# Optimization experiments

Measured on AMD Instinct MI355X. Metric: run time of the kernel, lower is better.

Reference implementation:

```python
import jax, jax.numpy as jnp
import numpy as np

N, NFEAT, NHID, NCLASS = 10000, 512, 64, 10
ALPHA = 0.2


def setup_inputs() -> dict:
    key = jax.random.key(0)
    ks = jax.random.split(key, 8)
    x = jax.random.normal(ks[0], (N, NFEAT), dtype=jnp.float32)
    adj1 = jax.random.uniform(ks[1], (N, N), dtype=jnp.float32) / N  # row-normalized-ish
    adj2 = jax.random.uniform(ks[2], (N, N), dtype=jnp.float32) / N
    # GraphConvolution params (glorot-ish scale)
    W1 = jax.random.normal(ks[3], (NFEAT, NHID), dtype=jnp.float32) * (1.0 / np.sqrt(NFEAT))
    b1 = jnp.zeros((NHID,), dtype=jnp.float32)
    W2 = jax.random.normal(ks[4], (NFEAT, NHID), dtype=jnp.float32) * (1.0 / np.sqrt(NFEAT))
    b2 = jnp.zeros((NHID,), dtype=jnp.float32)
    attn_w = jax.random.normal(ks[5], (NHID, 1), dtype=jnp.float32) * (1.0 / np.sqrt(NHID))
    cluster = jax.random.normal(ks[6], (NCLASS, NHID), dtype=jnp.float32)
    return {"x": x, "adj1": adj1, "adj2": adj2, "W1": W1, "b1": b1,
            "W2": W2, "b2": b2, "attn_w": attn_w, "cluster": cluster}


def reference(x, adj1, adj2, W1, b1, W2, b2, attn_w, cluster):
    # Two GCN branches: output = adj @ (x @ W) + b
    emb1 = adj1 @ (x @ W1) + b1  # [N, H]
    emb2 = adj2 @ (x @ W2) + b2  # [N, H]
    z = jnp.stack([emb1, emb2], axis=1)            # [N, 2, H]
    # tiny 2-way attention fusion
    w = z @ attn_w                                  # [N, 2, 1]
    beta = jax.nn.softmax(w, axis=1)                # softmax over the 2 views
    emb = jnp.sum(beta * z, axis=1)                 # [N, H]
    # DEC cluster assignment (faithful to the original, including the
    # second power and the /2, which the row-normalization cancels)
    d2 = jnp.sum((emb[:, None, :] - cluster[None, :, :]) ** 2, axis=2)  # [N, K]
    q = 1.0 / (1.0 + d2 / ALPHA)
    q = q ** ((ALPHA + 1.0) / 2.0)
    q = q ** (ALPHA + 1.0) / 2.0
    q = q / jnp.sum(q, axis=1, keepdims=True)
    return emb, q
```

## Files before the change

### kernel.cpp

```cpp
#include <hip/hip_runtime.h>
#include <math.h>

#define NROWS 10000
#define FEAT  512
#define NHID  64
#define NCLS  10
#define YT_STRIDE 10240
#define KB_PAD 320
#define TK    128
#define NSPLIT 4
#define TILES_PER_SPLIT 20

typedef __attribute__((ext_vector_type(8))) short short8;
typedef __attribute__((ext_vector_type(4))) float f32x4;

__device__ __forceinline__ short f2bf(float f) {
  union { float f; unsigned u; } v; v.f = f;
  unsigned r = v.u + 0x7fffu + ((v.u >> 16) & 1u);
  return (short)(r >> 16);
}

__device__ __forceinline__ float wsum64(float v) {
#pragma unroll
  for (int off = 32; off > 0; off >>= 1) v += __shfl_xor(v, off, 64);
  return v;
}

__device__ __forceinline__ void gload16(const void* g, void* l) {
  __builtin_amdgcn_global_load_lds(
      (const __attribute__((address_space(1))) unsigned int*)g,
      (__attribute__((address_space(3))) unsigned int*)l, 16, 0, 0);
}

__global__ __launch_bounds__(256) void prep_w(const float* __restrict__ W1,
                                              const float* __restrict__ W2,
                                              unsigned short* __restrict__ Wt1,
                                              unsigned short* __restrict__ Wt2) {
  int i = blockIdx.x * 256 + threadIdx.x;
  if (i >= FEAT * NHID) return;
  int k = i >> 6, h = i & 63;
  Wt1[h * FEAT + k] = (unsigned short)f2bf(W1[i]);
  Wt2[h * FEAT + k] = (unsigned short)f2bf(W2[i]);
}

__global__ __launch_bounds__(256) void gemm_xw(const float* __restrict__ x,
                                               const unsigned short* __restrict__ Wt1,
                                               const unsigned short* __restrict__ Wt2,
                                               unsigned short* __restrict__ Yt1,
                                               unsigned short* __restrict__ Yt2) {
  const int lane = threadIdx.x & 63;
  const int wave = threadIdx.x >> 6;
  const int job = blockIdx.x * 4 + wave;
  if (job >= 1250) return;
  const int br = (job >= 625) ? 1 : 0;
  const int tile = job - 625 * br;
  const unsigned short* Wt = br ? Wt2 : Wt1;
  unsigned short* Yt       = br ? Yt2 : Yt1;
  const int rowbase = tile * 16;
  const int r16 = lane & 15, g = lane >> 4, ga = g * 8;

  const float* arow = x + (size_t)(rowbase + r16) * FEAT + ga;
  const unsigned short* bp = Wt + (size_t)r16 * FEAT + ga;

  f32x4 acc[4];
#pragma unroll
  for (int t = 0; t < 4; ++t) acc[t] = (f32x4){0.f, 0.f, 0.f, 0.f};

#pragma unroll
  for (int kb = 0; kb < FEAT / 32; ++kb) {
    const int k0 = kb * 32;
    const f32x4* ap = (const f32x4*)(arow + k0);
    f32x4 a0 = ap[0], a1 = ap[1];
    short8 af;
    af[0] = f2bf(a0[0]); af[1] = f2bf(a0[1]); af[2] = f2bf(a0[2]); af[3] = f2bf(a0[3]);
    af[4] = f2bf(a1[0]); af[5] = f2bf(a1[1]); af[6] = f2bf(a1[2]); af[7] = f2bf(a1[3]);
#pragma unroll
    for (int t = 0; t < 4; ++t) {
      short8 bf = *(const short8*)(bp + (size_t)t * 16 * FEAT + k0);
      acc[t] = __builtin_amdgcn_mfma_f32_16x16x32_bf16(af, bf, acc[t], 0, 0, 0);
    }
  }
  const int sw = (r16 & 7) << 3;
#pragma unroll
  for (int t = 0; t < 4; ++t)
#pragma unroll
    for (int rr = 0; rr < 4; ++rr) {
      const int col = t * 16 + r16;
      const int row = rowbase + g * 4 + rr;
      Yt[(size_t)col * YT_STRIDE + (row ^ sw)] = (unsigned short)f2bf(acc[t][rr]);
    }
}

__global__ __launch_bounds__(256, 2) void gemm_adj(const float* __restrict__ adj1,
                                                   const float* __restrict__ adj2,
                                                   const unsigned short* __restrict__ Yt1,
                                                   const unsigned short* __restrict__ Yt2,
                                                   float* __restrict__ Ep) {
  __shared__ __attribute__((aligned(16))) float          Asm[2][32 * TK];
  __shared__ __attribute__((aligned(16))) unsigned short Bsm[2][64 * TK];

  const int sp = blockIdx.y;
  const int br = blockIdx.z;
  const float* adj         = br ? adj2 : adj1;
  const unsigned short* Yt = br ? Yt2 : Yt1;
  float* E = Ep + (size_t)(br * NSPLIT + sp) * NROWS * NHID;
  const int k_base = sp * (TILES_PER_SPLIT * TK);
  const int blockrow = blockIdx.x * 32;

  const int lane = threadIdx.x & 63;
  const int wave = threadIdx.x >> 6;

  const int ar_in = wave * 8 + (lane >> 5);
  const int a_lin = (lane & 31) * 4;
  const int b_cl = lane >> 4;
  const int b_el = (lane & 15) * 8;

  const int wr = wave >> 1, wc = wave & 1;
  const int r16 = lane & 15, g = lane >> 4;
  const int arow_t = wr * 16 + r16;
  const int aswz = (arow_t & 7) << 2;
  const int swb = (r16 & 7) << 3;

  f32x4 accL = (f32x4){0.f, 0.f, 0.f, 0.f};
  f32x4 accH = accL;

  auto STAGE = [&](int tt) {
    const int k0 = k_base + tt * TK;
    const int bufi = tt & 1;
#pragma unroll
    for (int j = 0; j < 4; ++j) {
      const int rt = ar_in + 2 * j;
      const int gr = min(blockrow + rt, NROWS - 1);
      const int fsrc = a_lin ^ ((gr & 7) << 2);
      const float* src = adj + (size_t)gr * NROWS + min(k0 + fsrc, NROWS - 4);
      gload16(src, &Asm[bufi][(wave * 8 + 2 * j) * TK]);
    }
#pragma unroll
    for (int j = 0; j < 4; ++j) {
      const int c0 = wave * 16 + j * 4;
      const unsigned short* src =
          Yt + (size_t)(c0 + b_cl) * YT_STRIDE + (k0 + b_el);
      gload16(src, &Bsm[bufi][c0 * TK]);
    }
  };

  auto COMPUTE = [&](int tt) {
    const int bufi = tt & 1;
    const int colL = wc * 32 + r16;
#pragma unroll
    for (int s = 0; s < TK / 32; ++s) {
      const int kx = s * 32 + g * 8;
      const float* abase = &Asm[bufi][arow_t * TK];
      f32x4 a0 = *(const f32x4*)(abase + (kx ^ aswz));
      f32x4 a1 = *(const f32x4*)(abase + ((kx + 4) ^ aswz));
      short8 bL = *(const short8*)&Bsm[bufi][colL * TK + (kx ^ swb)];
      short8 bH = *(const short8*)&Bsm[bufi][(colL + 16) * TK + (kx ^ swb)];
      short8 af;
      af[0] = f2bf(a0[0]); af[1] = f2bf(a0[1]); af[2] = f2bf(a0[2]); af[3] = f2bf(a0[3]);
      af[4] = f2bf(a1[0]); af[5] = f2bf(a1[1]); af[6] = f2bf(a1[2]); af[7] = f2bf(a1[3]);
      accL = __builtin_amdgcn_mfma_f32_16x16x32_bf16(af, bL, accL, 0, 0, 0);
      accH = __builtin_amdgcn_mfma_f32_16x16x32_bf16(af, bH, accH, 0, 0, 0);
    }
  };

  STAGE(0);
#pragma unroll 2
  for (int t = 0; t < TILES_PER_SPLIT - 1; ++t) {
    STAGE(t + 1);
    asm volatile("s_waitcnt vmcnt(8)" ::: "memory");
    __builtin_amdgcn_sched_barrier(0);
    __builtin_amdgcn_s_barrier();
    __builtin_amdgcn_sched_barrier(0);
    COMPUTE(t);
    __builtin_amdgcn_s_barrier();
  }
  asm volatile("s_waitcnt vmcnt(0)" ::: "memory");
  __builtin_amdgcn_sched_barrier(0);
  __builtin_amdgcn_s_barrier();
  __builtin_amdgcn_sched_barrier(0);
  COMPUTE(TILES_PER_SPLIT - 1);

#pragma unroll
  for (int rr = 0; rr < 4; ++rr) {
    const int grow = blockrow + wr * 16 + g * 4 + rr;
    if (grow < NROWS) {
      float* e = E + (size_t)grow * NHID + wc * 32 + r16;
      e[0]  = accL[rr];
      e[16] = accH[rr];
    }
  }
}

__global__ __launch_bounds__(256) void gemm_adj_dyn(const float* __restrict__ adj1,
                                                    const float* __restrict__ adj2,
                                                    const unsigned short* __restrict__ Yt1,
                                                    const unsigned short* __restrict__ Yt2,
                                                    float* __restrict__ Ep,
                                                    int nsplit, int chunk) {
  const int sp = blockIdx.y;
  const int br = blockIdx.z;
  const float* adj          = br ? adj2 : adj1;
  const unsigned short* Yt  = br ? Yt2 : Yt1;
  float* E = Ep + (size_t)(br * nsplit + sp) * NROWS * NHID;

  const int kb_begin = sp * chunk;
  const int kb_end   = min(kb_begin + chunk, KB_PAD);

  const int lane = threadIdx.x & 63;
  const int wave = threadIdx.x >> 6;
  const int rowbase = blockIdx.x * 64 + wave * 16;
  if (rowbase >= NROWS) return;
  const int r = lane & 15;
  const int g = lane >> 4;
  const int ga = g * 8;
  const int sw = (r & 7) << 3;

  const float* arow = adj + (size_t)(rowbase + r) * NROWS;

  f32x4 acc0 = (f32x4){0.f, 0.f, 0.f, 0.f};
  f32x4 acc1 = acc0, acc2 = acc0, acc3 = acc0;

#pragma unroll 4
  for (int kb = kb_begin; kb < kb_end; ++kb) {
    const int k0 = kb * 32;
    const int kc = min(k0 + ga, 9992);
    const int ks = (k0 + ga) ^ sw;
    const f32x4* ap = (const f32x4*)(arow + kc);
    f32x4 a0 = ap[0], a1 = ap[1];
    short8 af;
    af[0] = f2bf(a0[0]); af[1] = f2bf(a0[1]); af[2] = f2bf(a0[2]); af[3] = f2bf(a0[3]);
    af[4] = f2bf(a1[0]); af[5] = f2bf(a1[1]); af[6] = f2bf(a1[2]); af[7] = f2bf(a1[3]);
    short8 bf0 = *(const short8*)(Yt + (size_t)(0 * 16 + r) * YT_STRIDE + ks);
    short8 bf1 = *(const short8*)(Yt + (size_t)(1 * 16 + r) * YT_STRIDE + ks);
    short8 bf2 = *(const short8*)(Yt + (size_t)(2 * 16 + r) * YT_STRIDE + ks);
    short8 bf3 = *(const short8*)(Yt + (size_t)(3 * 16 + r) * YT_STRIDE + ks);
    acc0 = __builtin_amdgcn_mfma_f32_16x16x32_bf16(af, bf0, acc0, 0, 0, 0);
    acc1 = __builtin_amdgcn_mfma_f32_16x16x32_bf16(af, bf1, acc1, 0, 0, 0);
    acc2 = __builtin_amdgcn_mfma_f32_16x16x32_bf16(af, bf2, acc2, 0, 0, 0);
    acc3 = __builtin_amdgcn_mfma_f32_16x16x32_bf16(af, bf3, acc3, 0, 0, 0);
  }

  const size_t ebase = (size_t)(rowbase + g * 4) * NHID + r;
#pragma unroll
  for (int rr = 0; rr < 4; ++rr) {
    E[ebase + (size_t)rr * NHID +  0] = acc0[rr];
    E[ebase + (size_t)rr * NHID + 16] = acc1[rr];
    E[ebase + (size_t)rr * NHID + 32] = acc2[rr];
    E[ebase + (size_t)rr * NHID + 48] = acc3[rr];
  }
}

__global__ __launch_bounds__(256) void fuse(const float* __restrict__ Ep,
                                            int nsplit,
                                            const float* __restrict__ b1,
                                            const float* __restrict__ b2,
                                            const float* __restrict__ aw,
                                            const float* __restrict__ cl,
                                            float* __restrict__ out) {
  const int lane = threadIdx.x & 63;
  const int wave = threadIdx.x >> 6;
  const int row = blockIdx.x * 4 + wave;
  if (row >= NROWS) return;

  const size_t off = (size_t)row * NHID + lane;
  const size_t bstride = (size_t)nsplit * NROWS * NHID;
  float e1 = b1[lane], e2 = b2[lane];
  for (int s = 0; s < nsplit; ++s) {
    e1 += Ep[(size_t)s * NROWS * NHID + off];
    e2 += Ep[bstride + (size_t)s * NROWS * NHID + off];
  }

  float a = aw[lane];
  float w1 = wsum64(e1 * a);
  float w2 = wsum64(e2 * a);
  float m = fmaxf(w1, w2);
  float x1 = expf(w1 - m), x2 = expf(w2 - m);
  float inv = 1.0f / (x1 + x2);
  float emb = (x1 * e1 + x2 * e2) * inv;
  out[off] = emb;

  float myq = 0.f, qs = 0.f;
#pragma unroll
  for (int c = 0; c < NCLS; ++c) {
    float d = emb - cl[c * NHID + lane];
    float s = wsum64(d * d);
    float t = exp2f(-0.72f * log2f(fmaf(5.0f, s, 1.0f)));
    qs += t;
    if (lane == c) myq = t;
  }
  if (lane < NCLS) out[(size_t)NROWS * NHID + (size_t)row * NCLS + lane] = myq / qs;
}

extern "C" void kernel_launch(void* const* d_in, const int* in_sizes, int n_in,
                              void* d_out, int out_size, void* d_ws, size_t ws_size,
                              hipStream_t stream) {
  const float* x    = (const float*)d_in[0];
  const float* adj1 = (const float*)d_in[1];
  const float* adj2 = (const float*)d_in[2];
  const float* W1   = (const float*)d_in[3];
  const float* b1   = (const float*)d_in[4];
  const float* W2   = (const float*)d_in[5];
  const float* b2   = (const float*)d_in[6];
  const float* aw   = (const float*)d_in[7];
  const float* cl   = (const float*)d_in[8];
  float* out = (float*)d_out;

  char* ws = (char*)d_ws;
  unsigned short* Yt1 = (unsigned short*)(ws + 0);
  unsigned short* Yt2 = (unsigned short*)(ws + 1310720);
  unsigned short* Wt1 = (unsigned short*)(ws + 2621440);
  unsigned short* Wt2 = (unsigned short*)(ws + 2686976);
  float* Ep           = (float*)(ws + 2752512);

  const size_t fixed = 2752512;
  const size_t per_split = 2ull * NROWS * NHID * 4ull;
  const bool static_ok = ws_size >= fixed + (size_t)NSPLIT * per_split;

  hipMemsetAsync(Yt1, 0, 2 * 1310720, stream);
  prep_w<<<dim3(128), dim3(256), 0, stream>>>(W1, W2, Wt1, Wt2);
  gemm_xw<<<dim3(313), dim3(256), 0, stream>>>(x, Wt1, Wt2, Yt1, Yt2);

  if (static_ok) {
    gemm_adj<<<dim3(313, NSPLIT, 2), dim3(256), 0, stream>>>(adj1, adj2, Yt1, Yt2, Ep);
    fuse<<<dim3(2500), dim3(256), 0, stream>>>(Ep, NSPLIT, b1, b2, aw, cl, out);
  } else {
    int nsplit = 1;
    if (ws_size > fixed + per_split) {
      size_t s = (ws_size - fixed) / per_split;
      nsplit = (int)(s < 8 ? s : 8);
      if (nsplit < 1) nsplit = 1;
    }
    const int chunk = (KB_PAD + nsplit - 1) / nsplit;
    gemm_adj_dyn<<<dim3(157, nsplit, 2), dim3(256), 0, stream>>>(adj1, adj2, Yt1, Yt2,
                                                                 Ep, nsplit, chunk);
    fuse<<<dim3(2500), dim3(256), 0, stream>>>(Ep, nsplit, b1, b2, aw, cl, out);
  }
}
```

Before: 228.0 us.

## Load B operand directly into registers and double split-K with higher occupancy

The B operand (transposed bf16 XW) now goes straight from global memory into registers instead of being staged through LDS, which removes the Bsm buffer. The freed LDS is used to raise occupancy through launch bounds of 4 blocks per CU. Split-K doubles to 8 splits of 10 tiles each, giving more blocks. The costs are a larger partial-sum buffer and reduction, more B traffic because each wave loads its own columns, and a loss of overlap because the B loads for a tile are issued right before that tile is computed. The A swizzle now uses the local row instead of the global row, which gives the same result because blockrow is a multiple of 32, except for clamped rows past the end.

Measured after the change: 270.1 us. 18.5% more time.

```diff
diff --git a/kernel.cpp b/kernel.cpp
--- a/kernel.cpp
+++ b/kernel.cpp
@@ -8,8 +8,8 @@
 #define YT_STRIDE 10240
 #define KB_PAD 320
 #define TK    128
-#define NSPLIT 4
-#define TILES_PER_SPLIT 20
+#define NSPLIT 8
+#define TILES_PER_SPLIT 10
 
 typedef __attribute__((ext_vector_type(8))) short short8;
 typedef __attribute__((ext_vector_type(4))) float f32x4;
@@ -91,13 +91,12 @@
     }
 }
 
-__global__ __launch_bounds__(256, 2) void gemm_adj(const float* __restrict__ adj1,
+__global__ __launch_bounds__(256, 4) void gemm_adj(const float* __restrict__ adj1,
                                                    const float* __restrict__ adj2,
                                                    const unsigned short* __restrict__ Yt1,
                                                    const unsigned short* __restrict__ Yt2,
                                                    float* __restrict__ Ep) {
-  __shared__ __attribute__((aligned(16))) float          Asm[2][32 * TK];
-  __shared__ __attribute__((aligned(16))) unsigned short Bsm[2][64 * TK];
+  __shared__ __attribute__((aligned(16))) float Asm[2][32 * TK];
 
   const int sp = blockIdx.y;
   const int br = blockIdx.z;
@@ -110,10 +109,8 @@
   const int lane = threadIdx.x & 63;
   const int wave = threadIdx.x >> 6;
 
-  const int ar_in = wave * 8 + (lane >> 5);
+  const int l32 = lane >> 5;
   const int a_lin = (lane & 31) * 4;
-  const int b_cl = lane >> 4;
-  const int b_el = (lane & 15) * 8;
 
   const int wr = wave >> 1, wc = wave & 1;
   const int r16 = lane & 15, g = lane >> 4;
@@ -121,64 +118,72 @@
   const int aswz = (arow_t & 7) << 2;
   const int swb = (r16 & 7) << 3;
 
+  const int colL = wc * 32 + r16;
+  const unsigned short* ytL = Yt + (size_t)colL * YT_STRIDE;
+  const unsigned short* ytH = ytL + (size_t)16 * YT_STRIDE;
+
   f32x4 accL = (f32x4){0.f, 0.f, 0.f, 0.f};
   f32x4 accH = accL;
 
-  auto STAGE = [&](int tt) {
-    const int k0 = k_base + tt * TK;
-    const int bufi = tt & 1;
-#pragma unroll
-    for (int j = 0; j < 4; ++j) {
-      const int rt = ar_in + 2 * j;
-      const int gr = min(blockrow + rt, NROWS - 1);
-      const int fsrc = a_lin ^ ((gr & 7) << 2);
-      const float* src = adj + (size_t)gr * NROWS + min(k0 + fsrc, NROWS - 4);
-      gload16(src, &Asm[bufi][(wave * 8 + 2 * j) * TK]);
-    }
-#pragma unroll
-    for (int j = 0; j < 4; ++j) {
-      const int c0 = wave * 16 + j * 4;
-      const unsigned short* src =
-          Yt + (size_t)(c0 + b_cl) * YT_STRIDE + (k0 + b_el);
-      gload16(src, &Bsm[bufi][c0 * TK]);
-    }
-  };
-
-  auto COMPUTE = [&](int tt) {
-    const int bufi = tt & 1;
-    const int colL = wc * 32 + r16;
-#pragma unroll
-    for (int s = 0; s < TK / 32; ++s) {
-      const int kx = s * 32 + g * 8;
-      const float* abase = &Asm[bufi][arow_t * TK];
-      f32x4 a0 = *(const f32x4*)(abase + (kx ^ aswz));
-      f32x4 a1 = *(const f32x4*)(abase + ((kx + 4) ^ aswz));
-      short8 bL = *(const short8*)&Bsm[bufi][colL * TK + (kx ^ swb)];
-      short8 bH = *(const short8*)&Bsm[bufi][(colL + 16) * TK + (kx ^ swb)];
-      short8 af;
-      af[0] = f2bf(a0[0]); af[1] = f2bf(a0[1]); af[2] = f2bf(a0[2]); af[3] = f2bf(a0[3]);
-      af[4] = f2bf(a1[0]); af[5] = f2bf(a1[1]); af[6] = f2bf(a1[2]); af[7] = f2bf(a1[3]);
-      accL = __builtin_amdgcn_mfma_f32_16x16x32_bf16(af, bL, accL, 0, 0, 0);
-      accH = __builtin_amdgcn_mfma_f32_16x16x32_bf16(af, bH, accH, 0, 0, 0);
-    }
-  };
-
-  STAGE(0);
-#pragma unroll 2
+#define STAGE_A(tt) { const int k0s = k_base + (tt) * TK; const int bufs = (tt) & 1; \
+    _Pragma("unroll")                                                                 \
+    for (int j = 0; j < 4; ++j) {                                                     \
+      const int rt = wave * 8 + 2 * j + l32;                                          \
+      const int gr = min(blockrow + rt, NROWS - 1);                                   \
+      const int fsrc = a_lin ^ ((rt & 7) << 2);                                       \
+      const float* asrc = adj + (size_t)gr * NROWS + min(k0s + fsrc, NROWS - 4);      \
+      gload16(asrc, &Asm[bufs][(wave * 8 + 2 * j) * TK]);                             \
+    } }
+
+#define BLOAD(tt) { const int k0b = k_base + (tt) * TK;                               \
+    _Pragma("unroll")                                                                 \
+    for (int s = 0; s < 4; ++s) {                                                     \
+      const int off = k0b + ((s * 32 + g * 8) ^ swb);                                 \
+      BL[s] = *(const short8*)(ytL + off);                                            \
+      BH[s] = *(const short8*)(ytH + off);                                            \
+    } }
+
+#define COMPUTE(tt) { const int bufc = (tt) & 1;                                      \
+    const float* abase = &Asm[bufc][arow_t * TK];                                     \
+    _Pragma("unroll")                                                                 \
+    for (int s = 0; s < 4; ++s) {                                                     \
+      const int kx = s * 32 + g * 8;                                                  \
+      f32x4 a0 = *(const f32x4*)(abase + (kx ^ aswz));                                \
+      f32x4 a1 = *(const f32x4*)(abase + ((kx + 4) ^ aswz));                          \
+      short8 af;                                                                      \
+      af[0] = f2bf(a0[0]); af[1] = f2bf(a0[1]); af[2] = f2bf(a0[2]); af[3] = f2bf(a0[3]); \
+      af[4] = f2bf(a1[0]); af[5] = f2bf(a1[1]); af[6] = f2bf(a1[2]); af[7] = f2bf(a1[3]); \
+      accL = __builtin_amdgcn_mfma_f32_16x16x32_bf16(af, BL[s], accL, 0, 0, 0);       \
+      accH = __builtin_amdgcn_mfma_f32_16x16x32_bf16(af, BH[s], accH, 0, 0, 0);       \
+    } }
+
+  STAGE_A(0);
+#pragma unroll 1
   for (int t = 0; t < TILES_PER_SPLIT - 1; ++t) {
-    STAGE(t + 1);
-    asm volatile("s_waitcnt vmcnt(8)" ::: "memory");
+    short8 BL[4], BH[4];
+    BLOAD(t);
+    __builtin_amdgcn_sched_barrier(0);
+    asm volatile("" ::: "memory");
+    STAGE_A(t + 1);
+    asm volatile("s_waitcnt vmcnt(4)" ::: "memory");
     __builtin_amdgcn_sched_barrier(0);
     __builtin_amdgcn_s_barrier();
     __builtin_amdgcn_sched_barrier(0);
     COMPUTE(t);
     __builtin_amdgcn_s_barrier();
   }
-  asm volatile("s_waitcnt vmcnt(0)" ::: "memory");
-  __builtin_amdgcn_sched_barrier(0);
-  __builtin_amdgcn_s_barrier();
-  __builtin_amdgcn_sched_barrier(0);
-  COMPUTE(TILES_PER_SPLIT - 1);
+  {
+    short8 BL[4], BH[4];
+    BLOAD(TILES_PER_SPLIT - 1);
+    asm volatile("s_waitcnt vmcnt(0)" ::: "memory");
+    __builtin_amdgcn_sched_barrier(0);
+    __builtin_amdgcn_s_barrier();
+    __builtin_amdgcn_sched_barrier(0);
+    COMPUTE(TILES_PER_SPLIT - 1);
+  }
+#undef STAGE_A
+#undef BLOAD
+#undef COMPUTE
 
 #pragma unroll
   for (int rr = 0; rr < 4; ++rr) {
```
